# Optimization experiments

Hardware: AMD Instinct MI355X
Metric: run time of the kernel (lower is better)

Reference implementation:

```python
import jax, jax.numpy as jnp
import numpy as np

N_NODES = 50000
N_EDGES = 640000
F_IN = 64
EDGE_DIM = 16
HID = 128
N_LAYERS = 3
N_CLASSES = 2
NUM_GRAPHS = 64
BN_EPS = 1e-5


def setup_inputs() -> dict:
    key = jax.random.key(0)
    ks = jax.random.split(key, 20)
    s = 0.05
    inp = {
        "x": jax.random.normal(ks[0], (N_NODES, F_IN), dtype=jnp.float32),
        "edge_index": jax.random.randint(ks[1], (2, N_EDGES), 0, N_NODES, dtype=jnp.int32),
        "edge_attr": jax.random.normal(ks[2], (N_EDGES, EDGE_DIM), dtype=jnp.float32),
        "batch": jnp.sort(jax.random.randint(ks[3], (N_NODES,), 0, NUM_GRAPHS, dtype=jnp.int32)),
        # node encoder
        "enc_W": jax.random.normal(ks[4], (F_IN, HID), dtype=jnp.float32) * s,
        "enc_b": jnp.zeros((HID,), dtype=jnp.float32),
        # per-layer GINEConv params (stacked over layers)
        "edge_W": jax.random.normal(ks[5], (N_LAYERS, EDGE_DIM, HID), dtype=jnp.float32) * s,
        "edge_b": jnp.zeros((N_LAYERS, HID), dtype=jnp.float32),
        "mlp_W1": jax.random.normal(ks[6], (N_LAYERS, HID, HID), dtype=jnp.float32) * s,
        "mlp_b1": jnp.zeros((N_LAYERS, HID), dtype=jnp.float32),
        "mlp_W2": jax.random.normal(ks[7], (N_LAYERS, HID, HID), dtype=jnp.float32) * s,
        "mlp_b2": jnp.zeros((N_LAYERS, HID), dtype=jnp.float32),
        "bn_gamma": jnp.ones((N_LAYERS, HID), dtype=jnp.float32),
        "bn_beta": jnp.zeros((N_LAYERS, HID), dtype=jnp.float32),
        # classification head
        "head_W1": jax.random.normal(ks[8], (HID, HID), dtype=jnp.float32) * s,
        "head_b1": jnp.zeros((HID,), dtype=jnp.float32),
        "head_W2": jax.random.normal(ks[9], (HID, N_CLASSES), dtype=jnp.float32) * s,
        "head_b2": jnp.zeros((N_CLASSES,), dtype=jnp.float32),
    }
    return inp


def reference(x, edge_index, edge_attr, batch, enc_W, enc_b, edge_W, edge_b,
              mlp_W1, mlp_b1, mlp_W2, mlp_b2, bn_gamma, bn_beta,
              head_W1, head_b1, head_W2, head_b2):
    src, dst = edge_index[0], edge_index[1]  # message flows src -> dst
    h = x @ enc_W + enc_b  # [N, HID]
    for l in range(N_LAYERS):
        # GINEConv: msg = ReLU(x_src + Lin(edge_attr)); aggr = scatter_add at dst
        e = edge_attr @ edge_W[l] + edge_b[l]          # [E, HID]
        msg = jax.nn.relu(h[src] + e)                  # [E, HID]
        agg = jax.ops.segment_sum(msg, dst, num_segments=N_NODES)
        z = h + agg  # (1 + eps) * x + aggr, eps = 0
        # node MLP: Linear-ReLU-Linear
        z = jax.nn.relu(z @ mlp_W1[l] + mlp_b1[l]) @ mlp_W2[l] + mlp_b2[l]
        # BatchNorm1d (training-mode batch stats) + ReLU (dropout = identity)
        mean = jnp.mean(z, axis=0)
        var = jnp.var(z, axis=0)
        z = bn_gamma[l] * (z - mean) * jax.lax.rsqrt(var + BN_EPS) + bn_beta[l]
        h = jax.nn.relu(z)
    # global_add_pool over graphs
    g = jax.ops.segment_sum(h, batch, num_segments=NUM_GRAPHS)  # [G, HID]
    out = jax.nn.relu(g @ head_W1 + head_b1) @ head_W2 + head_b2
    return out  # [G, N_CLASSES]
```

## Files before the change

kernel.cpp:

```cpp
#include <hip/hip_runtime.h>
#include <hip/hip_bf16.h>

#define N_NODES 50000
#define N_EDGES 640000
#define F_IN 64
#define EDGE_DIM 16
#define HID 128
#define N_LAYERS 3
#define NUM_GRAPHS 64
#define BN_EPS 1e-5f

#define AGG_BLOCKS 2048
#define AGG_WAVES (AGG_BLOCKS * 4)

typedef __attribute__((ext_vector_type(8))) short short8;
typedef __attribute__((ext_vector_type(4))) float f32x4;
typedef __attribute__((ext_vector_type(2))) __fp16 half2v;

__device__ __forceinline__ float bfl(unsigned int u) {
    unsigned int v = u << 16; float f; __builtin_memcpy(&f, &v, 4); return f;
}
__device__ __forceinline__ float bfh(unsigned int u) {
    unsigned int v = u & 0xffff0000u; float f; __builtin_memcpy(&f, &v, 4); return f;
}
__device__ __forceinline__ unsigned int f2bf(float f) {
    unsigned int v; __builtin_memcpy(&v, &f, 4);
    v += 0x7fffu + ((v >> 16) & 1u);
    return v >> 16;
}
__device__ __forceinline__ unsigned int pack2(float lo, float hi) {
    return f2bf(lo) | (f2bf(hi) << 16);
}
__device__ __forceinline__ half2v u2h(unsigned int u) {
    half2v h; __builtin_memcpy(&h, &u, 4); return h;
}
__device__ __forceinline__ unsigned int pkh(float a, float b) {
    half2v h = __builtin_amdgcn_cvt_pkrtz(a, b);
    unsigned int u; __builtin_memcpy(&u, &h, 4); return u;
}

__global__ void k_hist(const int* __restrict__ dst, int* __restrict__ deg) {
    int e = blockIdx.x * 256 + threadIdx.x;
    atomicAdd(&deg[dst[e]], 1);
}

__global__ void k_blockred(const int* __restrict__ deg, int* __restrict__ bsums) {
    __shared__ int s[256];
    int i = blockIdx.x * 256 + threadIdx.x;
    int v = (i < N_NODES) ? deg[i] : 0;
    s[threadIdx.x] = v;
    __syncthreads();
    for (int off = 128; off > 0; off >>= 1) {
        if (threadIdx.x < off) s[threadIdx.x] += s[threadIdx.x + off];
        __syncthreads();
    }
    if (threadIdx.x == 0) bsums[blockIdx.x] = s[0];
}

__global__ void k_scan_bsums(int* __restrict__ bsums, int nb) {
    __shared__ int s[256];
    const int tid = threadIdx.x;
    const int v = (tid < nb) ? bsums[tid] : 0;
    s[tid] = v;
    __syncthreads();
    for (int off = 1; off < 256; off <<= 1) {
        int t = 0;
        if (tid >= off) t = s[tid - off];
        __syncthreads();
        s[tid] += t;
        __syncthreads();
    }
    if (tid < nb) bsums[tid] = s[tid] - v;
}

__global__ void k_scan_blocks(int* __restrict__ deg_rowptr, const int* __restrict__ bsums,
                              int* __restrict__ cursor) {
    __shared__ int s[256];
    int tid = threadIdx.x;
    int i = blockIdx.x * 256 + tid;
    int v = (i < N_NODES) ? deg_rowptr[i] : 0;
    s[tid] = v;
    __syncthreads();
    for (int off = 1; off < 256; off <<= 1) {
        int t = 0;
        if (tid >= off) t = s[tid - off];
        __syncthreads();
        s[tid] += t;
        __syncthreads();
    }
    int excl = s[tid] - v + bsums[blockIdx.x];
    if (i < N_NODES) {
        deg_rowptr[i] = excl;
        cursor[i] = excl;
    }
    if (i == N_NODES - 1) deg_rowptr[N_NODES] = N_EDGES;
}

__global__ void k_fill(const int* __restrict__ dst, int* __restrict__ cursor,
                       int* __restrict__ elist) {
    int e = blockIdx.x * 256 + threadIdx.x;
    int p = atomicAdd(&cursor[dst[e]], 1);
    elist[p] = e;
}

__global__ __launch_bounds__(256) void k_gather(const int* __restrict__ elist,
                                                const int* __restrict__ esrc,
                                                const float* __restrict__ eattr,
                                                int* __restrict__ src_s,
                                                uint4* __restrict__ eattr_h) {
    const int base = blockIdx.x * 1024;
    const int tid = threadIdx.x;
    int p[4], eid[4];
#pragma unroll
    for (int j = 0; j < 4; ++j) p[j] = base + tid + j * 256;
#pragma unroll
    for (int j = 0; j < 4; ++j) eid[j] = elist[p[j]];
    int sv[4];
#pragma unroll
    for (int j = 0; j < 4; ++j) sv[j] = esrc[eid[j]];
    float4 a[4][4];
#pragma unroll
    for (int j = 0; j < 4; ++j) {
        const float* ep = eattr + (size_t)eid[j] * EDGE_DIM;
        a[j][0] = *(const float4*)ep;
        a[j][1] = *(const float4*)(ep + 4);
        a[j][2] = *(const float4*)(ep + 8);
        a[j][3] = *(const float4*)(ep + 12);
    }
#pragma unroll
    for (int j = 0; j < 4; ++j) {
        src_s[p[j]] = sv[j];
        eattr_h[p[j] * 2] = make_uint4(pkh(a[j][0].x, a[j][0].y), pkh(a[j][0].z, a[j][0].w),
                                       pkh(a[j][1].x, a[j][1].y), pkh(a[j][1].z, a[j][1].w));
        eattr_h[p[j] * 2 + 1] = make_uint4(pkh(a[j][2].x, a[j][2].y), pkh(a[j][2].z, a[j][2].w),
                                           pkh(a[j][3].x, a[j][3].y), pkh(a[j][3].z, a[j][3].w));
    }
}

__global__ void k_pack(const float* __restrict__ W1, const float* __restrict__ W2,
                       const float* __restrict__ encW, const float* __restrict__ eW,
                       unsigned short* __restrict__ wp, unsigned short* __restrict__ wpe,
                       unsigned int* __restrict__ wek) {
    const int t = blockIdx.x * 256 + threadIdx.x;
    if (t < 12288) {
        const int mat = t >> 11;
        const int r = t & 2047;
        const int kstep = r >> 9;
        const int ntile = (r >> 6) & 7;
        const int lane = r & 63;
        const float* W = (mat < 3) ? (W1 + mat * 16384) : (W2 + (mat - 3) * 16384);
        const int kbase = kstep * 32 + ((lane >> 4) << 3);
        const int n = ntile * 16 + (lane & 15);
        unsigned int o[4];
#pragma unroll
        for (int jj = 0; jj < 4; ++jj)
            o[jj] = pack2(W[(kbase + 2 * jj) * HID + n], W[(kbase + 2 * jj + 1) * HID + n]);
        *(uint4*)(wp + (size_t)mat * 16384 + (((kstep << 3) + ntile) * 64 + lane) * 8) =
            make_uint4(o[0], o[1], o[2], o[3]);
    } else if (t < 13312) {
        const int r = t - 12288;
        const int kstep = r >> 9;
        const int ntile = (r >> 6) & 7;
        const int lane = r & 63;
        const int kbase = kstep * 32 + ((lane >> 4) << 3);
        const int n = ntile * 16 + (lane & 15);
        unsigned int o[4];
#pragma unroll
        for (int jj = 0; jj < 4; ++jj)
            o[jj] = pack2(encW[(kbase + 2 * jj) * HID + n], encW[(kbase + 2 * jj + 1) * HID + n]);
        *(uint4*)(wpe + (((kstep << 3) + ntile) * 64 + lane) * 8) =
            make_uint4(o[0], o[1], o[2], o[3]);
    } else {
        const int r = t - 13312;
        const int l = r >> 10;
        const int rr = r & 1023;
        const int kp = rr >> 7, f = rr & 127;
        const float a = eW[(l * EDGE_DIM + 2 * kp) * HID + f];
        const float b = eW[(l * EDGE_DIM + 2 * kp + 1) * HID + f];
        wek[r] = pkh(a, b);
    }
}

__global__ __launch_bounds__(256, 3) void k_encm(const float* __restrict__ x,
                                                 const unsigned short* __restrict__ wpe,
                                                 const float* __restrict__ b,
                                                 unsigned short* __restrict__ hb) {
    const int tid = threadIdx.x;
    const int w = tid >> 6, lane = tid & 63;
    const int q = lane >> 4, l15 = lane & 15;
    const int row0 = blockIdx.x * 64 + w * 16;
    const int ar = min(row0 + l15, N_NODES - 1);
    const float* xp = x + (size_t)ar * F_IN + q * 8;
    f32x4 acc[8];
#pragma unroll
    for (int nt = 0; nt < 8; ++nt) acc[nt] = (f32x4){0.f, 0.f, 0.f, 0.f};
#pragma unroll
    for (int ks = 0; ks < 2; ++ks) {
        const float4 v0 = *(const float4*)(xp + ks * 32);
        const float4 v1 = *(const float4*)(xp + ks * 32 + 4);
        unsigned int u[4] = {pack2(v0.x, v0.y), pack2(v0.z, v0.w),
                             pack2(v1.x, v1.y), pack2(v1.z, v1.w)};
        short8 a; __builtin_memcpy(&a, u, 16);
#pragma unroll
        for (int nt = 0; nt < 8; ++nt) {
            const short8 bf = *(const short8*)(wpe + (((ks << 3) + nt) * 64 + lane) * 8);
            acc[nt] = __builtin_amdgcn_mfma_f32_16x16x32_bf16(a, bf, acc[nt], 0, 0, 0);
        }
    }
    const int rowb = row0 + q * 4;
#pragma unroll
    for (int nt = 0; nt < 8; ++nt) {
        const float bias = b[nt * 16 + l15];
        const int cc = nt * 16 + l15;
#pragma unroll
        for (int reg = 0; reg < 4; ++reg) {
            const int r = rowb + reg;
            if (r < N_NODES)
                hb[(size_t)r * HID + cc] = (unsigned short)f2bf(acc[nt][reg] + bias);
        }
    }
}

__global__ __launch_bounds__(256, 2) void k_agg(const unsigned int* __restrict__ hb32,
                                                const int* __restrict__ src_s,
                                                const uint4* __restrict__ eattr_h,
                                                const unsigned int* __restrict__ wek,
                                                const float* __restrict__ be,
                                                const int* __restrict__ row_ptr,
                                                unsigned int* __restrict__ zb32) {
    const int lane = threadIdx.x & 63;
    const int wv = threadIdx.x >> 6;
    const int f2 = lane * 2;
    half2v wx[8], wy[8];
#pragma unroll
    for (int j = 0; j < 8; ++j) {
        wx[j] = u2h(wek[j * 128 + f2]);
        wy[j] = u2h(wek[j * 128 + f2 + 1]);
    }
    const float2 eb = *(const float2*)&be[f2];
    const int wgid = blockIdx.x * 4 + wv;

    for (int n = wgid; n < N_NODES; n += AGG_WAVES) {
        const int base = __builtin_amdgcn_readfirstlane(row_ptr[n]);
        const int deg = __builtin_amdgcn_readfirstlane(row_ptr[n + 1]) - base;

        const unsigned int hself = hb32[n * 64 + lane];
        float2 acc = make_float2(bfl(hself), bfh(hself));

        if (deg > 0) {
            const int* sp = src_s + base;
            const uint4* ep = eattr_h + (size_t)base * 2;
            const int last = deg - 1;
            const int nch = (deg + 3) >> 2;

            unsigned int huC[4], huN[4];
            uint4 eaC[4][2], eaN[4][2];
            int s2[4];
            {
                int s0[4], s1[4];
#pragma unroll
                for (int j = 0; j < 4; ++j) s0[j] = sp[min(j, last)];
#pragma unroll
                for (int j = 0; j < 4; ++j) huC[j] = hb32[s0[j] * 64 + lane];
#pragma unroll
                for (int j = 0; j < 4; ++j) s1[j] = sp[min(4 + j, last)];
                if (nch > 1) {
#pragma unroll
                    for (int j = 0; j < 4; ++j) huN[j] = hb32[s1[j] * 64 + lane];
                } else {
#pragma unroll
                    for (int j = 0; j < 4; ++j) huN[j] = 0u;
                }
#pragma unroll
                for (int j = 0; j < 4; ++j) {
                    const int e = min(j, last);
                    eaC[j][0] = ep[e * 2]; eaC[j][1] = ep[e * 2 + 1];
                }
#pragma unroll
                for (int j = 0; j < 4; ++j) s2[j] = sp[min(8 + j, last)];
            }
            for (int c = 0; c < nch; ++c) {
                unsigned int huNN[4] = {0u, 0u, 0u, 0u};
                if (c + 2 < nch) {
#pragma unroll
                    for (int j = 0; j < 4; ++j) huNN[j] = hb32[s2[j] * 64 + lane];
                }
                int s3[4];
#pragma unroll
                for (int j = 0; j < 4; ++j) s3[j] = sp[min((c + 3) * 4 + j, last)];
                if (c + 1 < nch) {
#pragma unroll
                    for (int j = 0; j < 4; ++j) {
                        const int e = min((c + 1) * 4 + j, last);
                        eaN[j][0] = ep[e * 2]; eaN[j][1] = ep[e * 2 + 1];
                    }
                }
                const int rem = deg - c * 4;
#pragma unroll
                for (int j = 0; j < 4; ++j) {
                    if (j < rem) {
                        const unsigned int* au = (const unsigned int*)&eaC[j][0];
                        float ex = eb.x, ey = eb.y;
#pragma unroll
                        for (int k = 0; k < 8; ++k) {
                            const half2v a = u2h(au[k]);
                            ex = __builtin_amdgcn_fdot2(a, wx[k], ex, false);
                            ey = __builtin_amdgcn_fdot2(a, wy[k], ey, false);
                        }
                        acc.x += fmaxf(bfl(huC[j]) + ex, 0.f);
                        acc.y += fmaxf(bfh(huC[j]) + ey, 0.f);
                    }
                }
                if (c + 1 < nch) {
#pragma unroll
                    for (int j = 0; j < 4; ++j) {
                        huC[j] = huN[j]; huN[j] = huNN[j];
                        eaC[j][0] = eaN[j][0]; eaC[j][1] = eaN[j][1];
                        s2[j] = s3[j];
                    }
                }
            }
        }
        zb32[n * 64 + lane] = pack2(acc.x, acc.y);
    }
}

#define Z1LD 136

__global__ __launch_bounds__(256, 3) void k_mlp(const unsigned short* __restrict__ zb,
                                                const unsigned short* __restrict__ w1p,
                                                const float* __restrict__ b1,
                                                const unsigned short* __restrict__ w2p,
                                                const float* __restrict__ b2,
                                                unsigned short* __restrict__ z2b,
                                                float* __restrict__ bn) {
    __shared__ unsigned short z1s[64 * Z1LD];
    __shared__ float redA[512];
    __shared__ float redB[512];
    const int tid = threadIdx.x;
    const int w = tid >> 6, lane = tid & 63;
    const int q = lane >> 4, l15 = lane & 15;
    const int row0 = blockIdx.x * 64 + w * 16;

    const int ar = min(row0 + l15, N_NODES - 1);
    const unsigned short* aptr = zb + (size_t)ar * HID + q * 8;

    f32x4 acc[8];
#pragma unroll
    for (int nt = 0; nt < 8; ++nt) acc[nt] = (f32x4){0.f, 0.f, 0.f, 0.f};

#pragma unroll
    for (int ks = 0; ks < 4; ++ks) {
        const short8 a = *(const short8*)(aptr + ks * 32);
#pragma unroll
        for (int nt = 0; nt < 8; ++nt) {
            const short8 b = *(const short8*)(w1p + (((ks << 3) + nt) * 64 + lane) * 8);
            acc[nt] = __builtin_amdgcn_mfma_f32_16x16x32_bf16(a, b, acc[nt], 0, 0, 0);
        }
    }
    {
        const int lr0 = w * 16 + q * 4;
#pragma unroll
        for (int nt = 0; nt < 8; ++nt) {
            const float bias = b1[nt * 16 + l15];
            const int cc = nt * 16 + l15;
#pragma unroll
            for (int reg = 0; reg < 4; ++reg) {
                const float v = fmaxf(acc[nt][reg] + bias, 0.f);
                z1s[(lr0 + reg) * Z1LD + cc] = (unsigned short)f2bf(v);
            }
        }
    }
#pragma unroll
    for (int nt = 0; nt < 8; ++nt) acc[nt] = (f32x4){0.f, 0.f, 0.f, 0.f};
    const unsigned short* a2p = &z1s[(w * 16 + l15) * Z1LD + q * 8];
#pragma unroll
    for (int ks = 0; ks < 4; ++ks) {
        const short8 a = *(const short8*)(a2p + ks * 32);
#pragma unroll
        for (int nt = 0; nt < 8; ++nt) {
            const short8 b = *(const short8*)(w2p + (((ks << 3) + nt) * 64 + lane) * 8);
            acc[nt] = __builtin_amdgcn_mfma_f32_16x16x32_bf16(a, b, acc[nt], 0, 0, 0);
        }
    }
    float s[8], sq[8];
    const int rowb = row0 + q * 4;
#pragma unroll
    for (int nt = 0; nt < 8; ++nt) {
        const float bias = b2[nt * 16 + l15];
        const int cc = nt * 16 + l15;
        float ls = 0.f, lq = 0.f;
#pragma unroll
        for (int reg = 0; reg < 4; ++reg) {
            const int r = rowb + reg;
            const float v = acc[nt][reg] + bias;
            if (r < N_NODES) {
                z2b[(size_t)r * HID + cc] = (unsigned short)f2bf(v);
                ls += v;
                lq = fmaf(v, v, lq);
            }
        }
        s[nt] = ls; sq[nt] = lq;
    }
#pragma unroll
    for (int nt = 0; nt < 8; ++nt) {
        s[nt] += __shfl_xor(s[nt], 16, 64);
        s[nt] += __shfl_xor(s[nt], 32, 64);
        sq[nt] += __shfl_xor(sq[nt], 16, 64);
        sq[nt] += __shfl_xor(sq[nt], 32, 64);
    }
    if (lane < 16) {
#pragma unroll
        for (int nt = 0; nt < 8; ++nt) {
            redA[w * 128 + nt * 16 + lane] = s[nt];
            redB[w * 128 + nt * 16 + lane] = sq[nt];
        }
    }
    __syncthreads();
    if (tid < 128) {
        float t = redA[tid] + redA[128 + tid] + redA[256 + tid] + redA[384 + tid];
        atomicAdd(&bn[tid], t);
    } else {
        const int c = tid - 128;
        float t = redB[c] + redB[128 + c] + redB[256 + c] + redB[384 + c];
        atomicAdd(&bn[128 + c], t);
    }
}

__global__ __launch_bounds__(256) void k_bnrelu(const unsigned short* __restrict__ z2b,
                                                const float* __restrict__ bn,
                                                const float* __restrict__ gamma,
                                                const float* __restrict__ beta,
                                                unsigned short* __restrict__ hb) {
    const int idx = (blockIdx.x * 256 + threadIdx.x) * 4;
    const int c = idx & 127;
    const float invN = 1.0f / (float)N_NODES;
    const uint2 zz = *(const uint2*)(z2b + idx);
    float o[4] = {bfl(zz.x), bfh(zz.x), bfl(zz.y), bfh(zz.y)};
#pragma unroll
    for (int k = 0; k < 4; ++k) {
        const float m = bn[c + k] * invN;
        float var = bn[128 + c + k] * invN - m * m;
        var = fmaxf(var, 0.f);
        const float r = rsqrtf(var + BN_EPS);
        o[k] = fmaxf(gamma[c + k] * (o[k] - m) * r + beta[c + k], 0.f);
    }
    *(uint2*)&hb[idx] = make_uint2(pack2(o[0], o[1]), pack2(o[2], o[3]));
}

__global__ void k_pool(const unsigned short* __restrict__ hb, const int* __restrict__ batch,
                       float* __restrict__ g) {
    const int f = threadIdx.x;
    const int n0 = blockIdx.x * 128;
    const int nend = min(n0 + 128, N_NODES);
    float acc = 0.f;
    int cur = batch[n0];
    for (int n = n0; n < nend; ++n) {
        const int bb = batch[n];
        if (bb != cur) {
            atomicAdd(&g[cur * HID + f], acc);
            acc = 0.f;
            cur = bb;
        }
        acc += bfl((unsigned int)hb[n * HID + f]);
    }
    atomicAdd(&g[cur * HID + f], acc);
}

__global__ void k_head1(const float* __restrict__ g, const float* __restrict__ W,
                        const float* __restrict__ b, float* __restrict__ g1) {
    const int idx = blockIdx.x * 256 + threadIdx.x;
    const int r = idx >> 7, c = idx & 127;
    float acc = b[c];
    for (int k = 0; k < 128; ++k) acc = fmaf(g[r * HID + k], W[k * HID + c], acc);
    g1[idx] = fmaxf(acc, 0.f);
}

__global__ void k_head2(const float* __restrict__ g1, const float* __restrict__ W,
                        const float* __restrict__ b, float* __restrict__ out) {
    const int idx = threadIdx.x;
    const int r = idx >> 1, c = idx & 1;
    float acc = b[c];
    for (int k = 0; k < 128; ++k) acc = fmaf(g1[r * HID + k], W[k * 2 + c], acc);
    out[idx] = acc;
}

extern "C" void kernel_launch(void* const* d_in, const int* in_sizes, int n_in,
                              void* d_out, int out_size, void* d_ws, size_t ws_size,
                              hipStream_t stream) {
    const float* x     = (const float*)d_in[0];
    const int*   ei    = (const int*)d_in[1];
    const float* eattr = (const float*)d_in[2];
    const int*   batch = (const int*)d_in[3];
    const float* encW  = (const float*)d_in[4];
    const float* encb  = (const float*)d_in[5];
    const float* eW    = (const float*)d_in[6];
    const float* eb    = (const float*)d_in[7];
    const float* W1    = (const float*)d_in[8];
    const float* b1    = (const float*)d_in[9];
    const float* W2    = (const float*)d_in[10];
    const float* b2    = (const float*)d_in[11];
    const float* gam   = (const float*)d_in[12];
    const float* bet   = (const float*)d_in[13];
    const float* hW1   = (const float*)d_in[14];
    const float* hb1   = (const float*)d_in[15];
    const float* hW2   = (const float*)d_in[16];
    const float* hb2   = (const float*)d_in[17];
    float* out = (float*)d_out;

    float* ws = (float*)d_ws;
    unsigned short* z2b = (unsigned short*)ws;
    float* bn  = ws + 3200000;
    float* g   = ws + 3200256;
    float* g1  = ws + 3208448;
    unsigned short* hb = (unsigned short*)(ws + 3216640);
    unsigned int* zb32 = (unsigned int*)(ws + 6416640);
    int* row_ptr = (int*)(ws + 11216640);
    int* cursor  = row_ptr + N_NODES + 1;
    int* elist   = cursor + N_NODES;
    int* bsums   = elist + N_EDGES;
    int* src_s   = bsums + 256;
    uint4* eattr_h = (uint4*)(ws + 12596900);
    unsigned short* wp  = (unsigned short*)(ws + 17716900);
    unsigned short* wpe = (unsigned short*)(ws + 17766100);
    unsigned int*   wek = (unsigned int*)(ws + 17770200);

    const int* esrc = ei;
    const int* edst = ei + N_EDGES;

    hipMemsetAsync(row_ptr, 0, (N_NODES + 1) * sizeof(int), stream);
    k_hist<<<N_EDGES / 256, 256, 0, stream>>>(edst, row_ptr);
    k_blockred<<<196, 256, 0, stream>>>(row_ptr, bsums);
    k_scan_bsums<<<1, 256, 0, stream>>>(bsums, 196);
    k_scan_blocks<<<196, 256, 0, stream>>>(row_ptr, bsums, cursor);
    k_fill<<<N_EDGES / 256, 256, 0, stream>>>(edst, cursor, elist);
    k_gather<<<N_EDGES / 1024, 256, 0, stream>>>(elist, esrc, eattr, src_s, eattr_h);

    k_pack<<<64, 256, 0, stream>>>(W1, W2, encW, eW, wp, wpe, wek);

    k_encm<<<782, 256, 0, stream>>>(x, wpe, encb, hb);

    for (int l = 0; l < N_LAYERS; ++l) {
        k_agg<<<AGG_BLOCKS, 256, 0, stream>>>((const unsigned int*)hb, src_s, eattr_h,
                                              wek + l * 1024, eb + l * HID, row_ptr, zb32);
        hipMemsetAsync(bn, 0, 256 * sizeof(float), stream);
        k_mlp<<<782, 256, 0, stream>>>((const unsigned short*)zb32,
                                       wp + (size_t)l * 16384, b1 + l * HID,
                                       wp + (size_t)(3 + l) * 16384, b2 + l * HID,
                                       z2b, bn);
        k_bnrelu<<<6250, 256, 0, stream>>>(z2b, bn, gam + l * HID, bet + l * HID, hb);
    }

    hipMemsetAsync(g, 0, NUM_GRAPHS * HID * sizeof(float), stream);
    k_pool<<<391, 128, 0, stream>>>(hb, batch, g);
    k_head1<<<32, 256, 0, stream>>>(g, hW1, hb1, g1);
    k_head2<<<1, 128, 0, stream>>>(g1, hW2, hb2, out);
}
```

Baseline: 608.9 us.

## Fuse BatchNorm+ReLU into next layer's aggregation and pooling, one wave per node

Drops the separate BN+ReLU kernel. The next aggregation kernel, or the final pooling kernel, now reads the raw MLP output and applies the BN scale/shift and ReLU on the fly. The aggregation grid changes from a fixed grid-stride loop to one wave per node (12500 blocks), and a sched_barrier is added in the gather loop. This removes a full read/write pass over the node features per layer. In exchange, BN is recomputed for every gathered neighbour, and many more blocks are launched.

```diff
diff --git a/kernel.cpp b/kernel.cpp
--- a/kernel.cpp
+++ b/kernel.cpp
@@ -9,9 +9,6 @@
 #define N_LAYERS 3
 #define NUM_GRAPHS 64
 #define BN_EPS 1e-5f
-
-#define AGG_BLOCKS 2048
-#define AGG_WAVES (AGG_BLOCKS * 4)
 
 typedef __attribute__((ext_vector_type(8))) short short8;
 typedef __attribute__((ext_vector_type(4))) float f32x4;
@@ -221,12 +218,16 @@
     }
 }
 
-__global__ __launch_bounds__(256, 2) void k_agg(const unsigned int* __restrict__ hb32,
+__global__ __launch_bounds__(256, 2) void k_agg(const unsigned int* __restrict__ in32,
                                                 const int* __restrict__ src_s,
                                                 const uint4* __restrict__ eattr_h,
                                                 const unsigned int* __restrict__ wek,
                                                 const float* __restrict__ be,
                                                 const int* __restrict__ row_ptr,
+                                                const float* __restrict__ bnst,
+                                                const float* __restrict__ gamma,
+                                                const float* __restrict__ beta,
+                                                const int bnmode,
                                                 unsigned int* __restrict__ zb32) {
     const int lane = threadIdx.x & 63;
     const int wv = threadIdx.x >> 6;
@@ -238,91 +239,106 @@
         wy[j] = u2h(wek[j * 128 + f2 + 1]);
     }
     const float2 eb = *(const float2*)&be[f2];
-    const int wgid = blockIdx.x * 4 + wv;
-
-    for (int n = wgid; n < N_NODES; n += AGG_WAVES) {
-        const int base = __builtin_amdgcn_readfirstlane(row_ptr[n]);
-        const int deg = __builtin_amdgcn_readfirstlane(row_ptr[n + 1]) - base;
-
-        const unsigned int hself = hb32[n * 64 + lane];
-        float2 acc = make_float2(bfl(hself), bfh(hself));
-
-        if (deg > 0) {
-            const int* sp = src_s + base;
-            const uint4* ep = eattr_h + (size_t)base * 2;
-            const int last = deg - 1;
-            const int nch = (deg + 3) >> 2;
-
-            unsigned int huC[4], huN[4];
-            uint4 eaC[4][2], eaN[4][2];
-            int s2[4];
-            {
-                int s0[4], s1[4];
-#pragma unroll
-                for (int j = 0; j < 4; ++j) s0[j] = sp[min(j, last)];
-#pragma unroll
-                for (int j = 0; j < 4; ++j) huC[j] = hb32[s0[j] * 64 + lane];
-#pragma unroll
-                for (int j = 0; j < 4; ++j) s1[j] = sp[min(4 + j, last)];
-                if (nch > 1) {
-#pragma unroll
-                    for (int j = 0; j < 4; ++j) huN[j] = hb32[s1[j] * 64 + lane];
-                } else {
-#pragma unroll
-                    for (int j = 0; j < 4; ++j) huN[j] = 0u;
+
+    float2 sc = make_float2(1.f, 1.f), sh = make_float2(0.f, 0.f);
+    float rlo = -3.4e38f;
+    if (bnmode) {
+        const float invN = 1.0f / (float)N_NODES;
+        const float m0 = bnst[f2] * invN, m1 = bnst[f2 + 1] * invN;
+        const float v0 = fmaxf(bnst[128 + f2] * invN - m0 * m0, 0.f);
+        const float v1 = fmaxf(bnst[128 + f2 + 1] * invN - m1 * m1, 0.f);
+        const float r0 = rsqrtf(v0 + BN_EPS), r1 = rsqrtf(v1 + BN_EPS);
+        sc = make_float2(gamma[f2] * r0, gamma[f2 + 1] * r1);
+        sh = make_float2(fmaf(-m0, sc.x, beta[f2]), fmaf(-m1, sc.y, beta[f2 + 1]));
+        rlo = 0.f;
+    }
+
+    const int n = blockIdx.x * 4 + wv;
+    const int base = __builtin_amdgcn_readfirstlane(row_ptr[n]);
+    const int deg = __builtin_amdgcn_readfirstlane(row_ptr[n + 1]) - base;
+
+    const unsigned int uself = in32[n * 64 + lane];
+    float2 acc = make_float2(fmaxf(fmaf(bfl(uself), sc.x, sh.x), rlo),
+                             fmaxf(fmaf(bfh(uself), sc.y, sh.y), rlo));
+
+    if (deg > 0) {
+        const int* sp = src_s + base;
+        const uint4* ep = eattr_h + (size_t)base * 2;
+        const int last = deg - 1;
+        const int nch = (deg + 3) >> 2;
+
+        unsigned int huC[4], huN[4];
+        uint4 eaC[4][2], eaN[4][2];
+        int s2[4];
+        {
+            int s0[4], s1[4];
+#pragma unroll
+            for (int j = 0; j < 4; ++j) s0[j] = sp[min(j, last)];
+#pragma unroll
+            for (int j = 0; j < 4; ++j) huC[j] = in32[s0[j] * 64 + lane];
+#pragma unroll
+            for (int j = 0; j < 4; ++j) s1[j] = sp[min(4 + j, last)];
+            if (nch > 1) {
+#pragma unroll
+                for (int j = 0; j < 4; ++j) huN[j] = in32[s1[j] * 64 + lane];
+            } else {
+#pragma unroll
+                for (int j = 0; j < 4; ++j) huN[j] = 0u;
+            }
+#pragma unroll
+            for (int j = 0; j < 4; ++j) {
+                const int e = min(j, last);
+                eaC[j][0] = ep[e * 2]; eaC[j][1] = ep[e * 2 + 1];
+            }
+#pragma unroll
+            for (int j = 0; j < 4; ++j) s2[j] = sp[min(8 + j, last)];
+        }
+        for (int c = 0; c < nch; ++c) {
+            unsigned int huNN[4] = {0u, 0u, 0u, 0u};
+            if (c + 2 < nch) {
+#pragma unroll
+                for (int j = 0; j < 4; ++j) huNN[j] = in32[s2[j] * 64 + lane];
+            }
+            int s3[4];
+#pragma unroll
+            for (int j = 0; j < 4; ++j) s3[j] = sp[min((c + 3) * 4 + j, last)];
+            if (c + 1 < nch) {
+#pragma unroll
+                for (int j = 0; j < 4; ++j) {
+                    const int e = min((c + 1) * 4 + j, last);
+                    eaN[j][0] = ep[e * 2]; eaN[j][1] = ep[e * 2 + 1];
                 }
+            }
+            __builtin_amdgcn_sched_barrier(0);
+            const int rem = deg - c * 4;
+#pragma unroll
+            for (int j = 0; j < 4; ++j) {
+                if (j < rem) {
+                    const unsigned int* au = (const unsigned int*)&eaC[j][0];
+                    float ex = eb.x, ey = eb.y;
+#pragma unroll
+                    for (int k = 0; k < 8; ++k) {
+                        const half2v a = u2h(au[k]);
+                        ex = __builtin_amdgcn_fdot2(a, wx[k], ex, false);
+                        ey = __builtin_amdgcn_fdot2(a, wy[k], ey, false);
+                    }
+                    const float hx = fmaxf(fmaf(bfl(huC[j]), sc.x, sh.x), rlo);
+                    const float hy = fmaxf(fmaf(bfh(huC[j]), sc.y, sh.y), rlo);
+                    acc.x += fmaxf(hx + ex, 0.f);
+                    acc.y += fmaxf(hy + ey, 0.f);
+                }
+            }
+            if (c + 1 < nch) {
 #pragma unroll
                 for (int j = 0; j < 4; ++j) {
-                    const int e = min(j, last);
-                    eaC[j][0] = ep[e * 2]; eaC[j][1] = ep[e * 2 + 1];
+                    huC[j] = huN[j]; huN[j] = huNN[j];
+                    eaC[j][0] = eaN[j][0]; eaC[j][1] = eaN[j][1];
+                    s2[j] = s3[j];
                 }
-#pragma unroll
-                for (int j = 0; j < 4; ++j) s2[j] = sp[min(8 + j, last)];
-            }
-            for (int c = 0; c < nch; ++c) {
-                unsigned int huNN[4] = {0u, 0u, 0u, 0u};
-                if (c + 2 < nch) {
-#pragma unroll
-                    for (int j = 0; j < 4; ++j) huNN[j] = hb32[s2[j] * 64 + lane];
-                }
-                int s3[4];
-#pragma unroll
-                for (int j = 0; j < 4; ++j) s3[j] = sp[min((c + 3) * 4 + j, last)];
-                if (c + 1 < nch) {
-#pragma unroll
-                    for (int j = 0; j < 4; ++j) {
-                        const int e = min((c + 1) * 4 + j, last);
-                        eaN[j][0] = ep[e * 2]; eaN[j][1] = ep[e * 2 + 1];
-                    }
-                }
-                const int rem = deg - c * 4;
-#pragma unroll
-                for (int j = 0; j < 4; ++j) {
-                    if (j < rem) {
-                        const unsigned int* au = (const unsigned int*)&eaC[j][0];
-                        float ex = eb.x, ey = eb.y;
-#pragma unroll
-                        for (int k = 0; k < 8; ++k) {
-                            const half2v a = u2h(au[k]);
-                            ex = __builtin_amdgcn_fdot2(a, wx[k], ex, false);
-                            ey = __builtin_amdgcn_fdot2(a, wy[k], ey, false);
-                        }
-                        acc.x += fmaxf(bfl(huC[j]) + ex, 0.f);
-                        acc.y += fmaxf(bfh(huC[j]) + ey, 0.f);
-                    }
-                }
-                if (c + 1 < nch) {
-#pragma unroll
-                    for (int j = 0; j < 4; ++j) {
-                        huC[j] = huN[j]; huN[j] = huNN[j];
-                        eaC[j][0] = eaN[j][0]; eaC[j][1] = eaN[j][1];
-                        s2[j] = s3[j];
-                    }
-                }
-            }
-        }
-        zb32[n * 64 + lane] = pack2(acc.x, acc.y);
-    }
+            }
+        }
+    }
+    zb32[n * 64 + lane] = pack2(acc.x, acc.y);
 }
 
 #define Z1LD 136
@@ -427,30 +443,17 @@
     }
 }
 
-__global__ __launch_bounds__(256) void k_bnrelu(const unsigned short* __restrict__ z2b,
-                                                const float* __restrict__ bn,
-                                                const float* __restrict__ gamma,
-                                                const float* __restrict__ beta,
-                                                unsigned short* __restrict__ hb) {
-    const int idx = (blockIdx.x * 256 + threadIdx.x) * 4;
-    const int c = idx & 127;
+__global__ void k_pool(const unsigned short* __restrict__ z2b, const int* __restrict__ batch,
+                       const float* __restrict__ bnst, const float* __restrict__ gamma,
+                       const float* __restrict__ beta, float* __restrict__ g) {
+    const int f = threadIdx.x;
     const float invN = 1.0f / (float)N_NODES;
-    const uint2 zz = *(const uint2*)(z2b + idx);
-    float o[4] = {bfl(zz.x), bfh(zz.x), bfl(zz.y), bfh(zz.y)};
-#pragma unroll
-    for (int k = 0; k < 4; ++k) {
-        const float m = bn[c + k] * invN;
-        float var = bn[128 + c + k] * invN - m * m;
-        var = fmaxf(var, 0.f);
-        const float r = rsqrtf(var + BN_EPS);
-        o[k] = fmaxf(gamma[c + k] * (o[k] - m) * r + beta[c + k], 0.f);
-    }
-    *(uint2*)&hb[idx] = make_uint2(pack2(o[0], o[1]), pack2(o[2], o[3]));
-}
-
-__global__ void k_pool(const unsigned short* __restrict__ hb, const int* __restrict__ batch,
-                       float* __restrict__ g) {
-    const int f = threadIdx.x;
+    const float m = bnst[f] * invN;
+    const float var = fmaxf(bnst[128 + f] * invN - m * m, 0.f);
+    const float r = rsqrtf(var + BN_EPS);
+    const float sc = gamma[f] * r;
+    const float sh = fmaf(-m, sc, beta[f]);
+
     const int n0 = blockIdx.x * 128;
     const int nend = min(n0 + 128, N_NODES);
     float acc = 0.f;
@@ -462,7 +465,8 @@
             acc = 0.f;
             cur = bb;
         }
-        acc += bfl((unsigned int)hb[n * HID + f]);
+        const float raw = bfl((unsigned int)z2b[n * HID + f]);
+        acc += fmaxf(fmaf(raw, sc, sh), 0.f);
     }
     atomicAdd(&g[cur * HID + f], acc);
 }
@@ -541,18 +545,22 @@
     k_encm<<<782, 256, 0, stream>>>(x, wpe, encb, hb);
 
     for (int l = 0; l < N_LAYERS; ++l) {
-        k_agg<<<AGG_BLOCKS, 256, 0, stream>>>((const unsigned int*)hb, src_s, eattr_h,
-                                              wek + l * 1024, eb + l * HID, row_ptr, zb32);
+        const unsigned int* in32 = (l == 0) ? (const unsigned int*)hb
+                                            : (const unsigned int*)z2b;
+        k_agg<<<12500, 256, 0, stream>>>(in32, src_s, eattr_h,
+                                         wek + l * 1024, eb + l * HID, row_ptr,
+                                         bn, gam + (l ? (l - 1) * HID : 0),
+                                         bet + (l ? (l - 1) * HID : 0),
+                                         (l > 0) ? 1 : 0, zb32);
         hipMemsetAsync(bn, 0, 256 * sizeof(float), stream);
         k_mlp<<<782, 256, 0, stream>>>((const unsigned short*)zb32,
                                        wp + (size_t)l * 16384, b1 + l * HID,
                                        wp + (size_t)(3 + l) * 16384, b2 + l * HID,
                                        z2b, bn);
-        k_bnrelu<<<6250, 256, 0, stream>>>(z2b, bn, gam + l * HID, bet + l * HID, hb);
     }
 
     hipMemsetAsync(g, 0, NUM_GRAPHS * HID * sizeof(float), stream);
-    k_pool<<<391, 128, 0, stream>>>(hb, batch, g);
+    k_pool<<<391, 128, 0, stream>>>(z2b, batch, bn, gam + 2 * HID, bet + 2 * HID, g);
     k_head1<<<32, 256, 0, stream>>>(g, hW1, hb1, g1);
     k_head2<<<1, 128, 0, stream>>>(g1, hW2, hb2, out);
 }
```

Result: faster. 571.1 us (-6.2%).
